# Optimization experiments

Measured on AMD Instinct MI355X. Metric: run time of the kernel, lower is better.

Reference implementation:

```python
import jax, jax.numpy as jnp
import numpy as np

B, S, W = 64, 128, 16
VOCAB, CVOCAB = 50000, 100
WDIM, CDIM, NF = 300, 50, 50
KS = [3, 4, 5]
HID, NLAYERS, NLAB = 256, 2, 5
COMB = WDIM + NF * len(KS)  # 450


def glorot(key, shape):
    fan_in, fan_out = shape[-2], shape[-1]
    lim = jnp.sqrt(6.0 / (fan_in + fan_out))
    return jax.random.uniform(key, shape, minval=-lim, maxval=lim, dtype=jnp.float32)


def setup_inputs() -> dict:
    key = jax.random.key(0)
    ks = jax.random.split(key, 32)
    word_ids = jax.random.randint(ks[0], (B, S), 1, VOCAB)
    char_ids = jax.random.randint(ks[1], (B, S, W), 1, CVOCAB)
    labels = jax.random.randint(ks[2], (B, S), 0, NLAB)
    lengths = jax.random.randint(ks[3], (B,), S // 2, S + 1)
    # embeddings
    word_emb = jax.random.normal(ks[4], (VOCAB, WDIM), jnp.float32) * 0.1
    word_emb = word_emb.at[0].set(0.0)
    char_emb = jax.random.normal(ks[5], (CVOCAB, CDIM), jnp.float32) * 0.1
    char_emb = char_emb.at[0].set(0.0)
    # char conv kernels: [ks, CDIM, NF] each, plus bias
    conv_w = [glorot(ks[6 + i], (k, CDIM, NF)) for i, k in enumerate(KS)]
    conv_b = [jnp.zeros((NF,), jnp.float32) for _ in KS]
    # LSTM params per layer per direction: W_ih [in,4H], W_hh [H,4H], b [4H]
    lstm = []
    kidx = 10
    in_dim = COMB
    for layer in range(NLAYERS):
        for d in range(2):
            Wih = glorot(ks[kidx], (in_dim, 4 * HID)); kidx += 1
            Whh = glorot(ks[kidx], (HID, 4 * HID)); kidx += 1
            b = jnp.zeros((4 * HID,), jnp.float32)
            lstm.extend([Wih, Whh, b])
        in_dim = 2 * HID
    out_w = glorot(ks[kidx], (2 * HID, NLAB)); kidx += 1
    out_b = jnp.zeros((NLAB,), jnp.float32)
    crf_start = jax.random.normal(ks[kidx], (NLAB,), jnp.float32) * 0.1; kidx += 1
    crf_end = jax.random.normal(ks[kidx], (NLAB,), jnp.float32) * 0.1; kidx += 1
    crf_trans = jax.random.normal(ks[kidx], (NLAB, NLAB), jnp.float32) * 0.1
    d = {
        'word_ids': word_ids, 'char_ids': char_ids, 'labels': labels, 'lengths': lengths,
        'word_emb': word_emb, 'char_emb': char_emb,
        'conv_w3': conv_w[0], 'conv_b3': conv_b[0],
        'conv_w4': conv_w[1], 'conv_b4': conv_b[1],
        'conv_w5': conv_w[2], 'conv_b5': conv_b[2],
        'out_w': out_w, 'out_b': out_b,
        'crf_start': crf_start, 'crf_end': crf_end, 'crf_trans': crf_trans,
    }
    names = ['Wih', 'Whh', 'b']
    i = 0
    for layer in range(NLAYERS):
        for dname in ['f', 'r']:
            for n in names:
                d[f'lstm_{n}_l{layer}{dname}'] = lstm[i]; i += 1
    return d


def _conv1d_same(x, w, b, pad):
    # x: [N, L, Cin], w: [k, Cin, Cout] -> [N, L_out, Cout]
    out = jax.lax.conv_general_dilated(x, w, window_strides=(1,), padding=[(pad, pad)],
                                       dimension_numbers=('NWC', 'WIO', 'NWC'))
    return out + b


def _lstm_dir(x, Wih, Whh, b, reverse):
    # x: [B, S, in] -> [B, S, H]; gate order i,f,g,o (torch convention)
    xg = jnp.einsum('bsi,ij->bsj', x, Wih) + b  # [B,S,4H]
    if reverse:
        xg = xg[:, ::-1]
    def step(carry, g):
        h, c = carry
        g = g + h @ Whh
        i, f, gg, o = jnp.split(g, 4, axis=-1)
        i, f, o = jax.nn.sigmoid(i), jax.nn.sigmoid(f), jax.nn.sigmoid(o)
        c = f * c + i * jnp.tanh(gg)
        h = o * jnp.tanh(c)
        return (h, c), h
    h0 = jnp.zeros((x.shape[0], HID), x.dtype)
    _, hs = jax.lax.scan(step, (h0, h0), jnp.swapaxes(xg, 0, 1))
    hs = jnp.swapaxes(hs, 0, 1)
    if reverse:
        hs = hs[:, ::-1]
    return hs


def reference(word_ids, char_ids, labels, lengths, word_emb, char_emb,
              conv_w3, conv_b3, conv_w4, conv_b4, conv_w5, conv_b5,
              out_w, out_b, crf_start, crf_end, crf_trans,
              lstm_Wih_l0f, lstm_Whh_l0f, lstm_b_l0f,
              lstm_Wih_l0r, lstm_Whh_l0r, lstm_b_l0r,
              lstm_Wih_l1f, lstm_Whh_l1f, lstm_b_l1f,
              lstm_Wih_l1r, lstm_Whh_l1r, lstm_b_l1r):
    # char CNN
    ce = char_emb[char_ids.reshape(-1, W)]  # [B*S, W, CDIM]
    pooled = []
    for w, b, k in [(conv_w3, conv_b3, 3), (conv_w4, conv_b4, 4), (conv_w5, conv_b5, 5)]:
        o = jax.nn.relu(_conv1d_same(ce, w, b, k // 2))
        pooled.append(jnp.max(o, axis=1))  # [B*S, NF]
    char_repr = jnp.concatenate(pooled, axis=-1).reshape(B, S, NF * len(KS))
    we = word_emb[word_ids]
    x = jnp.concatenate([we, char_repr], axis=-1)  # [B,S,COMB]
    # BiLSTM 2 layers (dropout disabled / eval mode)
    h_f = _lstm_dir(x, lstm_Wih_l0f, lstm_Whh_l0f, lstm_b_l0f, False)
    h_r = _lstm_dir(x, lstm_Wih_l0r, lstm_Whh_l0r, lstm_b_l0r, True)
    x = jnp.concatenate([h_f, h_r], axis=-1)
    h_f = _lstm_dir(x, lstm_Wih_l1f, lstm_Whh_l1f, lstm_b_l1f, False)
    h_r = _lstm_dir(x, lstm_Wih_l1r, lstm_Whh_l1r, lstm_b_l1r, True)
    x = jnp.concatenate([h_f, h_r], axis=-1)
    emissions = jnp.einsum('bsh,hl->bsl', x, out_w) + out_b  # [B,S,NLAB]
    # CRF NLL (pytorch-crf, batch_first, reduction='mean')
    mask = (jnp.arange(S)[None, :] < lengths[:, None])  # [B,S] bool
    maskf = mask.astype(emissions.dtype)
    tags = labels  # already in [0,NLAB)
    # numerator: score of gold path
    em_score = jnp.take_along_axis(emissions, tags[..., None], axis=-1)[..., 0]  # [B,S]
    num = crf_start[tags[:, 0]] + em_score[:, 0]
    trans_score = crf_trans[tags[:, :-1], tags[:, 1:]]  # [B,S-1]
    num = num + jnp.sum((trans_score + em_score[:, 1:]) * maskf[:, 1:], axis=1)
    last_idx = lengths - 1
    last_tag = jnp.take_along_axis(tags, last_idx[:, None], axis=1)[:, 0]
    num = num + crf_end[last_tag]
    # denominator: forward algorithm via scan
    alpha0 = crf_start + emissions[:, 0]  # [B,NLAB]
    def step(alpha, inp):
        em_t, m_t = inp  # [B,NLAB], [B]
        nxt = jax.nn.logsumexp(alpha[:, :, None] + crf_trans[None], axis=1) + em_t
        alpha = jnp.where(m_t[:, None], nxt, alpha)
        return alpha, None
    alpha, _ = jax.lax.scan(step, alpha0,
                            (jnp.swapaxes(emissions[:, 1:], 0, 1), jnp.swapaxes(mask[:, 1:], 0, 1)))
    denom = jax.nn.logsumexp(alpha + crf_end[None], axis=1)  # [B]
    llh = num - denom
    return -jnp.mean(llh)
```

## Files before the change

### kernel.cpp

```cpp
#include <hip/hip_runtime.h>
#include <hip/hip_fp16.h>
#include <math.h>
#include <stdint.h>

#define NB   64
#define NS   128
#define NW   16
#define CD   50
#define NF_  50
#define WD   300
#define COMB 450
#define K2P0 240
#define K2P1 256
#define HID  256
#define G4   1024
#define NLAB 5

#define WHH_SW4  (7.0f / 0.06846532f)
#define WHH_INV4 (1.0f / (WHH_SW4 * 7.0f))

typedef _Float16 h2_t __attribute__((ext_vector_type(2)));
typedef _Float16 v8h  __attribute__((ext_vector_type(8)));
typedef float    v16f __attribute__((ext_vector_type(16)));

__device__ __forceinline__ float sigf(float x)   { return 1.0f / (1.0f + __expf(-x)); }
__device__ __forceinline__ float tanhf_(float x) { return 1.0f - 2.0f / (__expf(2.0f * x) + 1.0f); }

__device__ __forceinline__ float dot2f(uint32_t a, uint32_t b, float c) {
#if __has_builtin(__builtin_amdgcn_fdot2)
    return __builtin_amdgcn_fdot2(__builtin_bit_cast(h2_t, a),
                                  __builtin_bit_cast(h2_t, b), c, false);
#else
    h2_t ah = __builtin_bit_cast(h2_t, a), bh = __builtin_bit_cast(h2_t, b);
    return c + (float)ah[0] * (float)bh[0] + (float)ah[1] * (float)bh[1];
#endif
}

__device__ __forceinline__ int sdot8f(uint32_t a, int b, int acc) {
#if __has_builtin(__builtin_amdgcn_sdot8)
    return __builtin_amdgcn_sdot8((int)a, b, acc, false);
#else
#pragma unroll
    for (int i = 0; i < 8; ++i) {
        int av = ((int)(a << (28 - 4 * i))) >> 28;
        int bv = ((int)(((uint32_t)b) << (28 - 4 * i))) >> 28;
        acc += av * bv;
    }
    return acc;
#endif
}

__device__ __forceinline__ uint32_t packh2(float lo, float hi) {
    __half l = __float2half(lo), h = __float2half(hi);
    return ((uint32_t)__half_as_ushort(h) << 16) | (uint32_t)__half_as_ushort(l);
}

__global__ __launch_bounds__(256) void pack_convw(
    const float* __restrict__ w3, const float* __restrict__ w4,
    const float* __restrict__ w5, uint32_t* __restrict__ cwp)
{
    int idx = blockIdx.x * 256 + threadIdx.x;
    if (idx >= 15000) return;
    const float* W; int rel;
    if (idx < 3750)       { W = w3; rel = idx; }
    else if (idx < 8750)  { W = w4; rel = idx - 3750; }
    else                  { W = w5; rel = idx - 8750; }
    int t = rel / 1250, rem = rel - t * 1250;
    int c2 = rem / 50, f = rem - c2 * 50;
    float lo = W[(size_t)t * (CD * NF_) + (2 * c2) * NF_ + f];
    float hi = W[(size_t)t * (CD * NF_) + (2 * c2 + 1) * NF_ + f];
    cwp[idx] = packh2(lo, hi);
}

__global__ __launch_bounds__(256) void cnn_embed2(
    const int* __restrict__ word_ids, const int* __restrict__ char_ids,
    const float* __restrict__ word_emb, const float* __restrict__ char_emb,
    const uint32_t* __restrict__ cwp,
    const float* __restrict__ b3, const float* __restrict__ b4,
    const float* __restrict__ b5, uint32_t* __restrict__ x0p)
{
    __shared__ uint32_t cep[4][NW][25];
    __shared__ float cv[4][152];
    int tid  = threadIdx.x;
    int g    = tid >> 6;
    int lane = tid & 63;
    int pos  = blockIdx.x * 4 + g;

    const int* cid = char_ids + (size_t)pos * NW;
    for (int idx = lane; idx < NW * 25; idx += 64) {
        int w  = idx / 25;
        int c2 = idx - w * 25;
        const float* e = char_emb + (size_t)cid[w] * CD + 2 * c2;
        cep[g][w][c2] = packh2(e[0], e[1]);
    }
    {
        int wid = word_ids[pos];
        const float* src = word_emb + (size_t)wid * WD;
        uint32_t* dst = x0p + (size_t)pos * K2P0;
        for (int idx = lane; idx < 150; idx += 64) {
            float2 v = *(const float2*)(src + 2 * idx);
            dst[idx] = packh2(v.x, v.y);
        }
        for (int idx = lane; idx < 15; idx += 64) dst[225 + idx] = 0;
    }
    __syncthreads();

    int f = lane;
    if (f < NF_) {
        float a3[16], a4[17], a5[16];
        float bb3 = b3[f], bb4 = b4[f], bb5 = b5[f];
#pragma unroll
        for (int p = 0; p < 16; ++p) { a3[p] = bb3; a5[p] = bb5; }
#pragma unroll
        for (int p = 0; p < 17; ++p) a4[p] = bb4;

        for (int c2 = 0; c2 < 25; ++c2) {
            uint32_t w3r[3], w4r[4], w5r[5];
#pragma unroll
            for (int t = 0; t < 3; ++t) w3r[t] = cwp[(t * 25 + c2) * NF_ + f];
#pragma unroll
            for (int t = 0; t < 4; ++t) w4r[t] = cwp[3750 + (t * 25 + c2) * NF_ + f];
#pragma unroll
            for (int t = 0; t < 5; ++t) w5r[t] = cwp[8750 + (t * 25 + c2) * NF_ + f];
#pragma unroll
            for (int ip = 0; ip < 16; ++ip) {
                uint32_t v = cep[g][ip][c2];
#pragma unroll
                for (int t = 0; t < 3; ++t) { int p = ip + 1 - t; if (p >= 0 && p < 16) a3[p] = dot2f(v, w3r[t], a3[p]); }
#pragma unroll
                for (int t = 0; t < 4; ++t) { int p = ip + 2 - t; if (p >= 0 && p < 17) a4[p] = dot2f(v, w4r[t], a4[p]); }
#pragma unroll
                for (int t = 0; t < 5; ++t) { int p = ip + 2 - t; if (p >= 0 && p < 16) a5[p] = dot2f(v, w5r[t], a5[p]); }
            }
        }
        float m3 = 0.f, m4 = 0.f, m5 = 0.f;
#pragma unroll
        for (int p = 0; p < 16; ++p) m3 = fmaxf(m3, a3[p]);
#pragma unroll
        for (int p = 0; p < 17; ++p) m4 = fmaxf(m4, a4[p]);
#pragma unroll
        for (int p = 0; p < 16; ++p) m5 = fmaxf(m5, a5[p]);
        cv[g][f] = m3; cv[g][50 + f] = m4; cv[g][100 + f] = m5;
    }
    __syncthreads();
    {
        uint32_t* dst = x0p + (size_t)pos * K2P0 + 150;
        for (int idx = lane; idx < 75; idx += 64)
            dst[idx] = packh2(cv[g][2 * idx], cv[g][2 * idx + 1]);
    }
}

__global__ __launch_bounds__(256) void pack_wih_all(
    const float* __restrict__ W0f, const float* __restrict__ W0r,
    const float* __restrict__ W1f, const float* __restrict__ W1r,
    uint32_t* __restrict__ P0f, uint32_t* __restrict__ P0r,
    uint32_t* __restrict__ P1f, uint32_t* __restrict__ P1r)
{
    int layer = blockIdx.z;
    int K   = layer ? 512 : COMB;
    int K2P = layer ? K2P1 : K2P0;
    const float* W = layer ? (blockIdx.y ? W1r : W1f) : (blockIdx.y ? W0r : W0f);
    uint32_t* P    = layer ? (blockIdx.y ? P1r : P1f) : (blockIdx.y ? P0r : P0f);

    int idx = blockIdx.x * 256 + threadIdx.x;
    if (idx >= K2P * 1024) return;
    int n = idx & 1023, kp = idx >> 10;
    uint32_t v = 0;
    if (2 * kp + 1 < K) {
        __half l = __float2half(W[(size_t)(2 * kp) * 1024 + n]);
        __half h = __float2half(W[(size_t)(2 * kp + 1) * 1024 + n]);
        v = ((uint32_t)__half_as_ushort(h) << 16) | (uint32_t)__half_as_ushort(l);
    }
    P[((size_t)(kp >> 2) * 1024 + n) * 4 + (kp & 3)] = v;
}

__global__ __launch_bounds__(256) void pack_whh_i4(
    const float* __restrict__ W0, const float* __restrict__ W1,
    const float* __restrict__ W2, const float* __restrict__ W3,
    uint32_t* __restrict__ Q0, uint32_t* __restrict__ Q1,
    uint32_t* __restrict__ Q2, uint32_t* __restrict__ Q3)
{
    int idx = blockIdx.x * 256 + threadIdx.x;
    if (idx >= 32768) return;
    const float* W; uint32_t* Q;
    switch (blockIdx.y) {
        case 0:  W = W0; Q = Q0; break;
        case 1:  W = W1; Q = Q1; break;
        case 2:  W = W2; Q = Q2; break;
        default: W = W3; Q = Q3; break;
    }
    int m = idx & 3, col = (idx >> 2) & 1023, iq = idx >> 12;
    int kbase = (iq * 4 + m) * 8;
    uint32_t out = 0;
#pragma unroll
    for (int j = 0; j < 8; ++j) {
        float w = W[(size_t)(kbase + j) * G4 + col];
        int q = (int)rintf(w * WHH_SW4);
        q = q < -7 ? -7 : (q > 7 ? 7 : q);
        out |= ((uint32_t)(q & 0xF)) << (4 * j);
    }
    Q[idx] = out;
}

__global__ __launch_bounds__(256) void gemm_mfma(
    const uint32_t* __restrict__ Ap, int K2,
    const uint32_t* __restrict__ Wpf, const uint32_t* __restrict__ Wpr,
    const float* __restrict__ bf, const float* __restrict__ br,
    float* __restrict__ Cf, float* __restrict__ Cr)
{
    int by  = blockIdx.y;
    int dir = by >> 4;
    int n0  = (by & 15) * 64;
    int m0  = blockIdx.x * 128;
    const uint32_t* Wp = dir ? Wpr : Wpf;
    const float* bias  = dir ? br : bf;
    float* C           = dir ? Cr : Cf;

    int tid = threadIdx.x;
    int w = tid >> 6, l = tid & 63;
    int l31 = l & 31, lk = l >> 5;

    const uint32_t* arow = Ap + (size_t)(m0 + w * 32 + l31) * K2 + lk * 4;
    const uint4*    bq0  = (const uint4*)(Wp) + (size_t)lk * 1024 + n0 + l31;

    v16f acc0 = {}, acc1 = {};

    for (int kp0 = 0; kp0 < K2; kp0 += 8) {
        uint4 av = *(const uint4*)(arow + kp0);
        const uint4* bq = bq0 + (size_t)(kp0 >> 2) * 1024;
        uint4 b0v = bq[0];
        uint4 b1v = bq[32];
        v8h af = __builtin_bit_cast(v8h, av);
        acc0 = __builtin_amdgcn_mfma_f32_32x32x16_f16(af, __builtin_bit_cast(v8h, b0v), acc0, 0, 0, 0);
        acc1 = __builtin_amdgcn_mfma_f32_32x32x16_f16(af, __builtin_bit_cast(v8h, b1v), acc1, 0, 0, 0);
    }

#pragma unroll
    for (int r = 0; r < 16; ++r) {
        int row = m0 + w * 32 + (r & 3) + 8 * (r >> 2) + 4 * lk;
        int c0 = n0 + l31, c1 = n0 + 32 + l31;
        C[(size_t)row * G4 + c0] = acc0[r] + bias[c0];
        C[(size_t)row * G4 + c1] = acc1[r] + bias[c1];
    }
}

__global__ __launch_bounds__(512, 1) void lstm_rec11(
    const float* __restrict__ xg_f, const float* __restrict__ xg_r,
    const uint32_t* __restrict__ Qf, const uint32_t* __restrict__ Qr,
    uint32_t* __restrict__ outp)
{
    int bid = blockIdx.x;
    int b = bid >> 1, d = bid & 1;
    const float* xg = d ? xg_r : xg_f;
    const uint4* Q4 = (const uint4*)(d ? Qr : Qf);

    __shared__ uint32_t hp8[32];
    __shared__ float gates[G4];
    __shared__ alignas(16) uint4 Tl[8 * 1024];

    int t = threadIdx.x;
    int lane = t & 63;

    for (int i = t; i < 8 * 1024; i += 512) Tl[i] = Q4[i];
    if (t < 32) hp8[t] = 0;
    float cst = 0.f;
    __syncthreads();

    for (int s = 0; s < NS; ++s) {
        int te = d ? (NS - 1 - s) : s;
        int row = b * NS + te;
        size_t r0 = (size_t)row * G4;
        float xA = xg[r0 + t];
        float xB = xg[r0 + 512 + t];

        int hreg = (int)hp8[lane & 31];
        int a0 = 0, a1 = 0;

#pragma unroll
        for (int iq = 0; iq < 8; ++iq) {
            uint4 wa = Tl[iq * 1024 + t];
            uint4 wb = Tl[iq * 1024 + t + 512];
            int h0 = __builtin_amdgcn_readlane(hreg, 4 * iq);
            int h1 = __builtin_amdgcn_readlane(hreg, 4 * iq + 1);
            int h2 = __builtin_amdgcn_readlane(hreg, 4 * iq + 2);
            int h3 = __builtin_amdgcn_readlane(hreg, 4 * iq + 3);
            a0 = sdot8f(wa.x, h0, a0); a0 = sdot8f(wa.y, h1, a0);
            a0 = sdot8f(wa.z, h2, a0); a0 = sdot8f(wa.w, h3, a0);
            a1 = sdot8f(wb.x, h0, a1); a1 = sdot8f(wb.y, h1, a1);
            a1 = sdot8f(wb.z, h2, a1); a1 = sdot8f(wb.w, h3, a1);
        }

        gates[t]       = (float)a0 * WHH_INV4 + xA;
        gates[t + 512] = (float)a1 * WHH_INV4 + xB;
        __syncthreads();
        if (t < 256) {
            int j = t;
            float gi = gates[j];
            float gf = gates[256 + j];
            float gg = gates[512 + j];
            float go = gates[768 + j];
            float ii = sigf(gi), ff = sigf(gf), g2 = tanhf_(gg), oo = sigf(go);
            cst = ff * cst + ii * g2;
            float h = oo * tanhf_(cst);
            int q = (int)rintf(h * 7.0f);
            q = q < -7 ? -7 : (q > 7 ? 7 : q);
            int qx = __shfl_xor(q, 1);
            float hx = __shfl_xor(h, 1);
            if (!(t & 1)) {
                ((unsigned char*)hp8)[j >> 1] =
                    (unsigned char)((q & 0xF) | ((qx & 0xF) << 4));
                outp[(size_t)row * 256 + d * 128 + (j >> 1)] = packh2(h, hx);
            }
        }
        __syncthreads();
    }
}

__global__ __launch_bounds__(256) void emis_kernel(
    const uint32_t* __restrict__ x2p, const float* __restrict__ ow,
    const float* __restrict__ ob, float* __restrict__ em)
{
    int i = blockIdx.x * blockDim.x + threadIdx.x;
    if (i >= NB * NS) return;
    const uint32_t* xr = x2p + (size_t)i * 256;
    float acc[NLAB];
#pragma unroll
    for (int l = 0; l < NLAB; ++l) acc[l] = ob[l];
    for (int p = 0; p < 256; ++p) {
        h2_t hv = __builtin_bit_cast(h2_t, xr[p]);
        float lo = (float)hv[0], hi = (float)hv[1];
        int k = 2 * p;
#pragma unroll
        for (int l = 0; l < NLAB; ++l)
            acc[l] += lo * ow[(size_t)k * NLAB + l] + hi * ow[(size_t)(k + 1) * NLAB + l];
    }
    float* e = em + (size_t)i * NLAB;
#pragma unroll
    for (int l = 0; l < NLAB; ++l) e[l] = acc[l];
}

__device__ __forceinline__ float lse5(const float* v) {
    float m = fmaxf(fmaxf(fmaxf(v[0], v[1]), fmaxf(v[2], v[3])), v[4]);
    float s = __expf(v[0] - m) + __expf(v[1] - m) + __expf(v[2] - m) +
              __expf(v[3] - m) + __expf(v[4] - m);
    return m + __logf(s);
}

__global__ __launch_bounds__(64) void crf_kernel(
    const float* __restrict__ em, const int* __restrict__ labels,
    const int* __restrict__ lengths, const float* __restrict__ cstart,
    const float* __restrict__ cend, const float* __restrict__ ctrans,
    float* __restrict__ outp)
{
    __shared__ float tr_s[25], st_s[5], en_s[5];
    int tid = threadIdx.x;
    if (tid < 25) tr_s[tid] = ctrans[tid];
    if (tid < 5)  { st_s[tid] = cstart[tid]; en_s[tid] = cend[tid]; }
    __syncthreads();

    int b = tid;
    int len = lengths[b];
    const int* tg = labels + (size_t)b * NS;
    const float* eb = em + (size_t)b * NS * NLAB;

    int prev = tg[0];
    float num = st_s[prev] + eb[prev];
    for (int t = 1; t < NS; ++t) {
        if (t < len) {
            int cur = tg[t];
            num += tr_s[prev * NLAB + cur] + eb[t * NLAB + cur];
            prev = cur;
        }
    }
    num += en_s[tg[len - 1]];

    float a[NLAB];
#pragma unroll
    for (int y = 0; y < NLAB; ++y) a[y] = st_s[y] + eb[y];
    for (int t = 1; t < NS; ++t) {
        if (t < len) {
            float na[NLAB];
#pragma unroll
            for (int y = 0; y < NLAB; ++y) {
                float v[NLAB];
#pragma unroll
                for (int x = 0; x < NLAB; ++x) v[x] = a[x] + tr_s[x * NLAB + y];
                na[y] = lse5(v) + eb[t * NLAB + y];
            }
#pragma unroll
            for (int y = 0; y < NLAB; ++y) a[y] = na[y];
        }
    }
    float v[NLAB];
#pragma unroll
    for (int y = 0; y < NLAB; ++y) v[y] = a[y] + en_s[y];
    float denom = lse5(v);

    float llh = num - denom;
#pragma unroll
    for (int off = 32; off > 0; off >>= 1) llh += __shfl_down(llh, off);
    if (tid == 0) outp[0] = -llh * (1.0f / 64.0f);
}

extern "C" void kernel_launch(void* const* d_in, const int* in_sizes, int n_in,
                              void* d_out, int out_size, void* d_ws, size_t ws_size,
                              hipStream_t stream)
{
    const int*   word_ids = (const int*)d_in[0];
    const int*   char_ids = (const int*)d_in[1];
    const int*   labels   = (const int*)d_in[2];
    const int*   lengths  = (const int*)d_in[3];
    const float* word_emb = (const float*)d_in[4];
    const float* char_emb = (const float*)d_in[5];
    const float* cw3 = (const float*)d_in[6];
    const float* cb3 = (const float*)d_in[7];
    const float* cw4 = (const float*)d_in[8];
    const float* cb4 = (const float*)d_in[9];
    const float* cw5 = (const float*)d_in[10];
    const float* cb5 = (const float*)d_in[11];
    const float* out_w = (const float*)d_in[12];
    const float* out_b = (const float*)d_in[13];
    const float* crf_start = (const float*)d_in[14];
    const float* crf_end   = (const float*)d_in[15];
    const float* crf_trans = (const float*)d_in[16];
    const float* Wih_l0f = (const float*)d_in[17];
    const float* Whh_l0f = (const float*)d_in[18];
    const float* b_l0f   = (const float*)d_in[19];
    const float* Wih_l0r = (const float*)d_in[20];
    const float* Whh_l0r = (const float*)d_in[21];
    const float* b_l0r   = (const float*)d_in[22];
    const float* Wih_l1f = (const float*)d_in[23];
    const float* Whh_l1f = (const float*)d_in[24];
    const float* b_l1f   = (const float*)d_in[25];
    const float* Wih_l1r = (const float*)d_in[26];
    const float* Whh_l1r = (const float*)d_in[27];
    const float* b_l1r   = (const float*)d_in[28];

    uint32_t* wsu = (uint32_t*)d_ws;
    uint32_t* x0p  = wsu;
    float*    xg_f = (float*)(wsu + 1966080);
    float*    xg_r = xg_f + 8388608;
    uint32_t* x1p  = (uint32_t*)(xg_r + 8388608);
    uint32_t* x2p  = x1p + 2097152;
    float*    em   = (float*)(x2p + 2097152);
    uint32_t* wp0f = (uint32_t*)(em + 40960);
    uint32_t* wp0r = wp0f + 245760;
    uint32_t* wp1f = wp0r + 245760;
    uint32_t* wp1r = wp1f + 262144;
    uint32_t* cwp  = wp1r + 262144;
    uint32_t* wh0f = x0p;
    uint32_t* wh0r = wh0f + 32768;
    uint32_t* wh1f = wh0r + 32768;
    uint32_t* wh1r = wh1f + 32768;

    pack_convw<<<59, 256, 0, stream>>>(cw3, cw4, cw5, cwp);

    cnn_embed2<<<2048, 256, 0, stream>>>(word_ids, char_ids, word_emb, char_emb,
                                         cwp, cb3, cb4, cb5, x0p);

    pack_wih_all<<<dim3(1024, 2, 2), 256, 0, stream>>>(
        Wih_l0f, Wih_l0r, Wih_l1f, Wih_l1r, wp0f, wp0r, wp1f, wp1r);

    dim3 gGemm(64, 32);
    gemm_mfma<<<gGemm, 256, 0, stream>>>(x0p, K2P0, wp0f, wp0r, b_l0f, b_l0r, xg_f, xg_r);

    pack_whh_i4<<<dim3(128, 4), 256, 0, stream>>>(Whh_l0f, Whh_l0r, Whh_l1f, Whh_l1r,
                                                  wh0f, wh0r, wh1f, wh1r);

    lstm_rec11<<<128, 512, 0, stream>>>(xg_f, xg_r, wh0f, wh0r, x1p);

    gemm_mfma<<<gGemm, 256, 0, stream>>>(x1p, K2P1, wp1f, wp1r, b_l1f, b_l1r, xg_f, xg_r);

    lstm_rec11<<<128, 512, 0, stream>>>(xg_f, xg_r, wh1f, wh1r, x2p);

    emis_kernel<<<32, 256, 0, stream>>>(x2p, out_w, out_b, em);
    crf_kernel<<<1, 64, 0, stream>>>(em, labels, lengths, crf_start, crf_end, crf_trans,
                                     (float*)d_out);
}
```

Measured before the change: 562.9 us.

## Keep half of recurrent weights in registers and stage conv weights in LDS

```diff
diff --git a/kernel.cpp b/kernel.cpp
--- a/kernel.cpp
+++ b/kernel.cpp
@@ -72,19 +72,21 @@
     cwp[idx] = packh2(lo, hi);
 }
 
-__global__ __launch_bounds__(256) void cnn_embed2(
+__global__ __launch_bounds__(512) void cnn_embed3(
     const int* __restrict__ word_ids, const int* __restrict__ char_ids,
     const float* __restrict__ word_emb, const float* __restrict__ char_emb,
     const uint32_t* __restrict__ cwp,
     const float* __restrict__ b3, const float* __restrict__ b4,
     const float* __restrict__ b5, uint32_t* __restrict__ x0p)
 {
-    __shared__ uint32_t cep[4][NW][25];
-    __shared__ float cv[4][152];
+    __shared__ uint32_t cws[15000];
+    __shared__ uint32_t cep[8][NW][25];
     int tid  = threadIdx.x;
     int g    = tid >> 6;
     int lane = tid & 63;
-    int pos  = blockIdx.x * 4 + g;
+    int pos  = blockIdx.x * 8 + g;
+
+    for (int i = tid; i < 15000; i += 512) cws[i] = cwp[i];
 
     const int* cid = char_ids + (size_t)pos * NW;
     for (int idx = lane; idx < NW * 25; idx += 64) {
@@ -106,6 +108,7 @@
     __syncthreads();
 
     int f = lane;
+    float m3 = 0.f, m4 = 0.f, m5 = 0.f;
     if (f < NF_) {
         float a3[16], a4[17], a5[16];
         float bb3 = b3[f], bb4 = b4[f], bb5 = b5[f];
@@ -117,11 +120,11 @@
         for (int c2 = 0; c2 < 25; ++c2) {
             uint32_t w3r[3], w4r[4], w5r[5];
 #pragma unroll
-            for (int t = 0; t < 3; ++t) w3r[t] = cwp[(t * 25 + c2) * NF_ + f];
-#pragma unroll
-            for (int t = 0; t < 4; ++t) w4r[t] = cwp[3750 + (t * 25 + c2) * NF_ + f];
-#pragma unroll
-            for (int t = 0; t < 5; ++t) w5r[t] = cwp[8750 + (t * 25 + c2) * NF_ + f];
+            for (int t = 0; t < 3; ++t) w3r[t] = cws[(t * 25 + c2) * NF_ + f];
+#pragma unroll
+            for (int t = 0; t < 4; ++t) w4r[t] = cws[3750 + (t * 25 + c2) * NF_ + f];
+#pragma unroll
+            for (int t = 0; t < 5; ++t) w5r[t] = cws[8750 + (t * 25 + c2) * NF_ + f];
 #pragma unroll
             for (int ip = 0; ip < 16; ++ip) {
                 uint32_t v = cep[g][ip][c2];
@@ -133,20 +136,22 @@
                 for (int t = 0; t < 5; ++t) { int p = ip + 2 - t; if (p >= 0 && p < 16) a5[p] = dot2f(v, w5r[t], a5[p]); }
             }
         }
-        float m3 = 0.f, m4 = 0.f, m5 = 0.f;
 #pragma unroll
         for (int p = 0; p < 16; ++p) m3 = fmaxf(m3, a3[p]);
 #pragma unroll
         for (int p = 0; p < 17; ++p) m4 = fmaxf(m4, a4[p]);
 #pragma unroll
         for (int p = 0; p < 16; ++p) m5 = fmaxf(m5, a5[p]);
-        cv[g][f] = m3; cv[g][50 + f] = m4; cv[g][100 + f] = m5;
-    }
-    __syncthreads();
-    {
+    }
+    float m3x = __shfl_xor(m3, 1);
+    float m4x = __shfl_xor(m4, 1);
+    float m5x = __shfl_xor(m5, 1);
+    if (f < NF_ && !(f & 1)) {
+        int i = f >> 1;
         uint32_t* dst = x0p + (size_t)pos * K2P0 + 150;
-        for (int idx = lane; idx < 75; idx += 64)
-            dst[idx] = packh2(cv[g][2 * idx], cv[g][2 * idx + 1]);
+        dst[i]      = packh2(m3, m3x);
+        dst[25 + i] = packh2(m4, m4x);
+        dst[50 + i] = packh2(m5, m5x);
     }
 }
 
@@ -244,7 +249,7 @@
     }
 }
 
-__global__ __launch_bounds__(512, 1) void lstm_rec11(
+__global__ __launch_bounds__(512, 1) void lstm_rec12(
     const float* __restrict__ xg_f, const float* __restrict__ xg_r,
     const uint32_t* __restrict__ Qf, const uint32_t* __restrict__ Qr,
     uint32_t* __restrict__ outp)
@@ -256,12 +261,18 @@
 
     __shared__ uint32_t hp8[32];
     __shared__ float gates[G4];
-    __shared__ alignas(16) uint4 Tl[8 * 1024];
+    __shared__ alignas(16) uint4 Tl[4 * 1024];
 
     int t = threadIdx.x;
     int lane = t & 63;
 
-    for (int i = t; i < 8 * 1024; i += 512) Tl[i] = Q4[i];
+    uint4 rA[4], rB[4];
+#pragma unroll
+    for (int iq = 0; iq < 4; ++iq) {
+        rA[iq] = Q4[(size_t)iq * 1024 + t];
+        rB[iq] = Q4[(size_t)iq * 1024 + t + 512];
+    }
+    for (int i = t; i < 4 * 1024; i += 512) Tl[i] = Q4[4 * 1024 + i];
     if (t < 32) hp8[t] = 0;
     float cst = 0.f;
     __syncthreads();
@@ -277,13 +288,24 @@
         int a0 = 0, a1 = 0;
 
 #pragma unroll
-        for (int iq = 0; iq < 8; ++iq) {
-            uint4 wa = Tl[iq * 1024 + t];
-            uint4 wb = Tl[iq * 1024 + t + 512];
+        for (int iq = 0; iq < 4; ++iq) {
             int h0 = __builtin_amdgcn_readlane(hreg, 4 * iq);
             int h1 = __builtin_amdgcn_readlane(hreg, 4 * iq + 1);
             int h2 = __builtin_amdgcn_readlane(hreg, 4 * iq + 2);
             int h3 = __builtin_amdgcn_readlane(hreg, 4 * iq + 3);
+            a0 = sdot8f(rA[iq].x, h0, a0); a0 = sdot8f(rA[iq].y, h1, a0);
+            a0 = sdot8f(rA[iq].z, h2, a0); a0 = sdot8f(rA[iq].w, h3, a0);
+            a1 = sdot8f(rB[iq].x, h0, a1); a1 = sdot8f(rB[iq].y, h1, a1);
+            a1 = sdot8f(rB[iq].z, h2, a1); a1 = sdot8f(rB[iq].w, h3, a1);
+        }
+#pragma unroll
+        for (int iq2 = 0; iq2 < 4; ++iq2) {
+            uint4 wa = Tl[iq2 * 1024 + t];
+            uint4 wb = Tl[iq2 * 1024 + t + 512];
+            int h0 = __builtin_amdgcn_readlane(hreg, 16 + 4 * iq2);
+            int h1 = __builtin_amdgcn_readlane(hreg, 17 + 4 * iq2);
+            int h2 = __builtin_amdgcn_readlane(hreg, 18 + 4 * iq2);
+            int h3 = __builtin_amdgcn_readlane(hreg, 19 + 4 * iq2);
             a0 = sdot8f(wa.x, h0, a0); a0 = sdot8f(wa.y, h1, a0);
             a0 = sdot8f(wa.z, h2, a0); a0 = sdot8f(wa.w, h3, a0);
             a1 = sdot8f(wb.x, h0, a1); a1 = sdot8f(wb.y, h1, a1);
@@ -455,7 +477,7 @@
 
     pack_convw<<<59, 256, 0, stream>>>(cw3, cw4, cw5, cwp);
 
-    cnn_embed2<<<2048, 256, 0, stream>>>(word_ids, char_ids, word_emb, char_emb,
+    cnn_embed3<<<1024, 512, 0, stream>>>(word_ids, char_ids, word_emb, char_emb,
                                          cwp, cb3, cb4, cb5, x0p);
 
     pack_wih_all<<<dim3(1024, 2, 2), 256, 0, stream>>>(
@@ -467,11 +489,11 @@
     pack_whh_i4<<<dim3(128, 4), 256, 0, stream>>>(Whh_l0f, Whh_l0r, Whh_l1f, Whh_l1r,
                                                   wh0f, wh0r, wh1f, wh1r);
 
-    lstm_rec11<<<128, 512, 0, stream>>>(xg_f, xg_r, wh0f, wh0r, x1p);
+    lstm_rec12<<<128, 512, 0, stream>>>(xg_f, xg_r, wh0f, wh0r, x1p);
 
     gemm_mfma<<<gGemm, 256, 0, stream>>>(x1p, K2P1, wp1f, wp1r, b_l1f, b_l1r, xg_f, xg_r);
 
-    lstm_rec11<<<128, 512, 0, stream>>>(xg_f, xg_r, wh1f, wh1r, x2p);
+    lstm_rec12<<<128, 512, 0, stream>>>(xg_f, xg_r, wh1f, wh1r, x2p);
 
     emis_kernel<<<32, 256, 0, stream>>>(x2p, out_w, out_b, em);
     crf_kernel<<<1, 64, 0, stream>>>(em, labels, lengths, crf_start, crf_end, crf_trans,
```

After: 545.7 us. 1.03x faster.
